# Kernel tuning notes

Hardware: AMD Instinct MI355X
Metric: run time of the kernel (lower is better)

Reference implementation:

```python
import jax, jax.numpy as jnp
import numpy as np

NUM_NODES = 500000
EMBED_DIM = 128
BATCH = 50000
NUM_SAMPLE = 32


def setup_inputs() -> dict:
    key = jax.random.key(0)
    k1, k2 = jax.random.split(key)
    neighbors = jax.random.randint(k1, (BATCH, NUM_SAMPLE), 0, NUM_NODES, dtype=jnp.int64 if jax.config.jax_enable_x64 else jnp.int32)
    emb_weight = jax.random.normal(k2, (NUM_NODES, EMBED_DIM), dtype=jnp.float32)
    return {"neighbors": neighbors, "emb_weight": emb_weight}


def reference(neighbors, emb_weight):
    # Original: build one-hot mask [batch, unique], row-normalize by degree,
    # mask @ emb(unique)  ==  per-node mean of sampled neighbor embeddings.
    # Faithful fused form: gather then mean over the neighbor axis.
    neigh_feats = emb_weight[neighbors]            # [B, S, D] gather
    to_feats = jnp.mean(neigh_feats, axis=1)       # [B, D] segment-mean (fixed fan-out)
    return to_feats
```

## Files before the change

kernel.cpp:

```cpp
#include <hip/hip_runtime.h>
#include <hip/hip_bf16.h>


#define AGG_BATCH 50000
#define AGG_S 32
#define AGG_D2 64
#define AGG_WAVES_PER_BLOCK 4

__global__ __launch_bounds__(256) void mean_aggregator_49795850830175_kernel(
    const int* __restrict__ neighbors,
    const float2* __restrict__ emb,
    float2* __restrict__ out) {
  const int lane = threadIdx.x & 63;
  int row = blockIdx.x * AGG_WAVES_PER_BLOCK + (threadIdx.x >> 6);
  row = __builtin_amdgcn_readfirstlane(row);

  const int* __restrict__ nb = neighbors + (size_t)row * AGG_S;

  float acc_x = 0.f, acc_y = 0.f;
#pragma unroll
  for (int s = 0; s < AGG_S; ++s) {
    int idx = __builtin_amdgcn_readfirstlane(nb[s]);
    const float2 v = emb[(size_t)idx * AGG_D2 + lane];
    acc_x += v.x;
    acc_y += v.y;
  }

  const float inv = 1.0f / (float)AGG_S;
  float2 r;
  r.x = acc_x * inv;
  r.y = acc_y * inv;
  out[(size_t)row * AGG_D2 + lane] = r;
}

extern "C" void kernel_launch(void* const* d_in, const int* in_sizes, int n_in,
                              void* d_out, int out_size, void* d_ws, size_t ws_size,
                              hipStream_t stream) {
  const int* neighbors = (const int*)d_in[0];
  const float2* emb = (const float2*)d_in[1];
  float2* out = (float2*)d_out;

  const int grid = AGG_BATCH / AGG_WAVES_PER_BLOCK;
  mean_aggregator_49795850830175_kernel<<<grid, 256, 0, stream>>>(neighbors, emb, out);
}
```

Baseline: 398.8 us.

## Convert embedding table to fp16 in workspace before gathering

Adds a pre-pass that converts the full fp32 embedding table to fp16 in the workspace, then gathers half-width rows and accumulates in fp32. This halves the bytes per gathered row to reduce random-gather traffic. It adds a full-table read and write each call and loses precision in the inputs. It falls back to the direct fp32 gather when the workspace is too small.

```diff
diff --git a/kernel.cpp b/kernel.cpp
--- a/kernel.cpp
+++ b/kernel.cpp
@@ -1,45 +1,91 @@
 #include <hip/hip_runtime.h>
-#include <hip/hip_bf16.h>
+#include <hip/hip_fp16.h>
+#include <string.h>
 
 
 #define AGG_BATCH 50000
 #define AGG_S 32
-#define AGG_D2 64
-#define AGG_WAVES_PER_BLOCK 4
+#define AGG_NODES 500000
+#define AGG_D 128
+#define AGG_ELEMS ((size_t)AGG_NODES * AGG_D)
+#define AGG_WS_BYTES (AGG_ELEMS * 2)
+
+__global__ __launch_bounds__(256) void agg_convert_kernel(
+    const float4* __restrict__ in, uint4* __restrict__ out16) {
+  const size_t i = (size_t)blockIdx.x * 256 + threadIdx.x;
+  const float4 a = in[2 * i];
+  const float4 b = in[2 * i + 1];
+  const __half2 h0 = __floats2half2_rn(a.x, a.y);
+  const __half2 h1 = __floats2half2_rn(a.z, a.w);
+  const __half2 h2 = __floats2half2_rn(b.x, b.y);
+  const __half2 h3 = __floats2half2_rn(b.z, b.w);
+  uint4 o;
+  memcpy(&o.x, &h0, 4);
+  memcpy(&o.y, &h1, 4);
+  memcpy(&o.z, &h2, 4);
+  memcpy(&o.w, &h3, 4);
+  out16[i] = o;
+}
 
 __global__ __launch_bounds__(256) void mean_aggregator_49795850830175_kernel(
+    const int* __restrict__ neighbors,
+    const unsigned int* __restrict__ tab16,
+    float2* __restrict__ out) {
+  const int lane = threadIdx.x & 63;
+  int row = blockIdx.x * 4 + (threadIdx.x >> 6);
+  row = __builtin_amdgcn_readfirstlane(row);
+
+  const int* __restrict__ nb = neighbors + (size_t)row * AGG_S;
+
+  float ax = 0.f, ay = 0.f;
+#pragma unroll
+  for (int s = 0; s < AGG_S; ++s) {
+    const int idx = __builtin_amdgcn_readfirstlane(nb[s]);
+    const unsigned int v = tab16[(size_t)idx * (AGG_D / 2) + lane];
+    __half2 h;
+    memcpy(&h, &v, 4);
+    const float2 f = __half22float2(h);
+    ax += f.x;
+    ay += f.y;
+  }
+  const float inv = 1.0f / (float)AGG_S;
+  out[(size_t)row * (AGG_D / 2) + lane] = make_float2(ax * inv, ay * inv);
+}
+
+__global__ __launch_bounds__(256) void agg_direct_kernel(
     const int* __restrict__ neighbors,
     const float2* __restrict__ emb,
     float2* __restrict__ out) {
   const int lane = threadIdx.x & 63;
-  int row = blockIdx.x * AGG_WAVES_PER_BLOCK + (threadIdx.x >> 6);
+  int row = blockIdx.x * 4 + (threadIdx.x >> 6);
   row = __builtin_amdgcn_readfirstlane(row);
-
   const int* __restrict__ nb = neighbors + (size_t)row * AGG_S;
-
-  float acc_x = 0.f, acc_y = 0.f;
+  float ax = 0.f, ay = 0.f;
 #pragma unroll
   for (int s = 0; s < AGG_S; ++s) {
-    int idx = __builtin_amdgcn_readfirstlane(nb[s]);
-    const float2 v = emb[(size_t)idx * AGG_D2 + lane];
-    acc_x += v.x;
-    acc_y += v.y;
+    const int idx = __builtin_amdgcn_readfirstlane(nb[s]);
+    const float2 v = emb[(size_t)idx * (AGG_D / 2) + lane];
+    ax += v.x;
+    ay += v.y;
   }
-
   const float inv = 1.0f / (float)AGG_S;
-  float2 r;
-  r.x = acc_x * inv;
-  r.y = acc_y * inv;
-  out[(size_t)row * AGG_D2 + lane] = r;
+  out[(size_t)row * (AGG_D / 2) + lane] = make_float2(ax * inv, ay * inv);
 }
 
 extern "C" void kernel_launch(void* const* d_in, const int* in_sizes, int n_in,
                               void* d_out, int out_size, void* d_ws, size_t ws_size,
                               hipStream_t stream) {
   const int* neighbors = (const int*)d_in[0];
-  const float2* emb = (const float2*)d_in[1];
-  float2* out = (float2*)d_out;
+  const float* emb = (const float*)d_in[1];
 
-  const int grid = AGG_BATCH / AGG_WAVES_PER_BLOCK;
-  mean_aggregator_49795850830175_kernel<<<grid, 256, 0, stream>>>(neighbors, emb, out);
+  if (ws_size >= AGG_WS_BYTES) {
+    const int conv_grid = (int)(AGG_ELEMS / 8 / 256);
+    agg_convert_kernel<<<conv_grid, 256, 0, stream>>>(
+        (const float4*)emb, (uint4*)d_ws);
+    mean_aggregator_49795850830175_kernel<<<AGG_BATCH / 4, 256, 0, stream>>>(
+        neighbors, (const unsigned int*)d_ws, (float2*)d_out);
+  } else {
+    agg_direct_kernel<<<AGG_BATCH / 4, 256, 0, stream>>>(
+        neighbors, (const float2*)emb, (float2*)d_out);
+  }
 }
```

Result: slower. 415.8 us (+4.3%).
